# Performance work log

Hardware: AMD Instinct MI355X
Metric: run time of the kernel (lower is better)

The kernel has to match this reference:

```python
import jax, jax.numpy as jnp
import numpy as np

PUPIL = 256          # pupil / OPD grid size
OUTPUT_DIM = 64      # cropped PSF postage-stamp size
N_BINS = 8           # number of SED wavelength bins
BATCH = 16
# Static, wavelength-dependent diffraction padding sizes (phase_N per bin).
# In the original these come from packed_SED_data[:,0,:] but are constant in a FoV.
PHASE_NS = [1024, 988, 952, 918, 886, 856, 828, 802]


def setup_inputs() -> dict:
    key = jax.random.key(0)
    k1, k2, k3 = jax.random.split(key, 3)
    # OPD in meters: small wavefront errors (~lambda/10 rms)
    opd_batch = jax.random.normal(k1, (BATCH, PUPIL, PUPIL), dtype=jnp.float32) * 1e-7
    # Annular pupil: outer aperture with central obscuration (like Euclid/VIS optics)
    yy, xx = np.mgrid[:PUPIL, :PUPIL].astype(np.float32)
    c = (PUPIL - 1) / 2.0
    r = np.sqrt((xx - c) ** 2 + (yy - c) ** 2) / (PUPIL / 2.0)
    obscurations = jnp.asarray(((r <= 1.0) & (r >= 0.3)).astype(np.float32))
    # Observed wavelengths per bin, in meters (visible band)
    lambdas = jnp.linspace(0.55e-6, 0.9e-6, N_BINS).astype(jnp.float32)
    # Normalized SED weights
    sed = jax.random.uniform(k2, (N_BINS,), dtype=jnp.float32) + 0.1
    sed_norms = sed / jnp.sum(sed)
    return {
        "opd_batch": opd_batch,
        "obscurations": obscurations,
        "lambdas": lambdas,
        "sed_norms": sed_norms,
    }


def _mono_psf(opd, obsc, lam, phase_N, out_dim):
    """Batched monochromatic PSF: OPD -> phase -> padded FFT -> cropped |.|^2, unit-sum."""
    # opd: [B, p, p]; phase = exp(i * 2pi/lambda * opd) * obscurations
    pre_phase = (2.0 * jnp.pi / lam) * opd
    phase = (jnp.cos(pre_phase) + 1j * jnp.sin(pre_phase)).astype(jnp.complex64)
    phase = phase * obsc.astype(jnp.complex64)
    p = opd.shape[-1]
    pad_lo = (phase_N - p) // 2
    pad_hi = phase_N - p - pad_lo
    padded = jnp.pad(phase, ((0, 0), (pad_lo, pad_hi), (pad_lo, pad_hi)))  # [B, N, N]
    fft = jnp.fft.fftshift(jnp.fft.fft2(padded), axes=(-2, -1))
    psf = fft.real ** 2 + fft.imag ** 2  # |FFT|^2, float32
    start = phase_N // 2 - out_dim // 2
    psf = psf[:, start:start + out_dim, start:start + out_dim]  # central crop
    return psf / jnp.sum(psf, axis=(-2, -1), keepdims=True)


def reference(opd_batch, obscurations, lambdas, sed_norms):
    # Polychromatic PSF: SED-weighted sum of monochromatic PSFs over wavelength bins.
    # Loop is over the small fixed set of bins (distinct static FFT sizes);
    # each bin is fully vectorized over the batch.
    out = jnp.zeros((opd_batch.shape[0], OUTPUT_DIM, OUTPUT_DIM), dtype=jnp.float32)
    for b, phase_N in enumerate(PHASE_NS):
        out = out + sed_norms[b] * _mono_psf(
            opd_batch, obscurations, lambdas[b], phase_N, OUTPUT_DIM
        )
    return out
```

## Files before the change

### kernel.cpp

```cpp
#include <hip/hip_runtime.h>
#include <math.h>

#define PUPIL 256
#define OUT_DIM 64
#define N_BINS 8
#define BATCH 16

__constant__ int PHASE_NS_C[N_BINS] = {1024, 988, 952, 918, 886, 856, 828, 802};

typedef short bf16x8 __attribute__((ext_vector_type(8)));
typedef float f32x4  __attribute__((ext_vector_type(4)));
typedef int   i32x4  __attribute__((ext_vector_type(4)));

#define MFMA16(a, b, c) __builtin_amdgcn_mfma_f32_16x16x32_bf16((a), (b), (c), 0, 0, 0)

__device__ __forceinline__ short f2bf(float f) {
  unsigned u = __float_as_uint(f);
  u += 0x7FFFu + ((u >> 16) & 1u);
  return (short)(u >> 16);
}

__device__ __forceinline__ bf16x8 neg8(bf16x8 v) {
  i32x4 t = __builtin_bit_cast(i32x4, v);
  t ^= (int)0x80008000;
  return __builtin_bit_cast(bf16x8, t);
}


__global__ void wprep(short* __restrict__ Wr_t, short* __restrict__ Wi_t) {
  int idx = blockIdx.x * 256 + threadIdx.x;
  int n   = idx & 255;
  int k   = (idx >> 8) & 63;
  int bin = idx >> 14;
  int N = PHASE_NS_C[bin];
  int m = ((k - 32) * n) % N;
  if (m < 0) m += N;
  float ang = -6.283185307179586f * (float)m / (float)N;
  float s, c;
  sincosf(ang, &s, &c);
  Wr_t[idx] = f2bf(c);
  Wi_t[idx] = f2bf(s);
}

__global__ __launch_bounds__(256, 2) void stage1(
    const float* __restrict__ opd, const float* __restrict__ obsc,
    const float* __restrict__ lambdas,
    const short* __restrict__ Wr_t, const short* __restrict__ Wi_t,
    short* __restrict__ Gr_t, short* __restrict__ Gi_t)
{
  const int tid = threadIdx.x;
  const int yb = blockIdx.x, bin = blockIdx.y, b = blockIdx.z;
  const int bb = b * N_BINS + bin;
  const float w0 = 6.283185307179586f / lambdas[bin];

  __shared__ short Pr[64 * 32], Pi[64 * 32];

  const int wave = tid >> 6, lane = tid & 63;
  const int lr = lane & 15, lq = lane >> 4;

  f32x4 accR[4], accI[4];
  #pragma unroll
  for (int t = 0; t < 4; ++t) { accR[t] = (f32x4)0.0f; accI[t] = (f32x4)0.0f; }

  const int py = tid >> 2;
  const int px = (tid & 3) * 8;
  const float* opdrow = opd + ((size_t)b * PUPIL + (yb * 64 + py)) * PUPIL;
  const float* obsrow = obsc + (size_t)(yb * 64 + py) * PUPIL;

  const short* wrb = Wr_t + ((size_t)bin * 64 + wave * 16 + lr) * 256 + lq * 8;
  const short* wib = Wi_t + ((size_t)bin * 64 + wave * 16 + lr) * 256 + lq * 8;

  for (int xc = 0; xc < 8; ++xc) {
    const int xbase = xc * 32;
    float od[8], ob[8];
    *(float4*)&od[0] = *(const float4*)(opdrow + xbase + px);
    *(float4*)&od[4] = *(const float4*)(opdrow + xbase + px + 4);
    *(float4*)&ob[0] = *(const float4*)(obsrow + xbase + px);
    *(float4*)&ob[4] = *(const float4*)(obsrow + xbase + px + 4);
    bf16x8 vr, vi;
    #pragma unroll
    for (int j = 0; j < 8; ++j) {
      float s, c;
      __sincosf(w0 * od[j], &s, &c);
      vr[j] = f2bf(c * ob[j]);
      vi[j] = f2bf(s * ob[j]);
    }
    __syncthreads();
    *(bf16x8*)&Pr[py * 32 + px] = vr;
    *(bf16x8*)&Pi[py * 32 + px] = vi;
    const bf16x8 wr  = *(const bf16x8*)(wrb + xbase);
    const bf16x8 wi  = *(const bf16x8*)(wib + xbase);
    const bf16x8 nwi = neg8(wi);
    __syncthreads();

    #pragma unroll
    for (int t = 0; t < 4; ++t) {
      const bf16x8 pr = *(const bf16x8*)&Pr[(t * 16 + lr) * 32 + lq * 8];
      const bf16x8 pi = *(const bf16x8*)&Pi[(t * 16 + lr) * 32 + lq * 8];
      accR[t] = MFMA16(wr,  pr, accR[t]);
      accR[t] = MFMA16(nwi, pi, accR[t]);
      accI[t] = MFMA16(wr,  pi, accI[t]);
      accI[t] = MFMA16(wi,  pr, accI[t]);
    }
  }

  #pragma unroll
  for (int t = 0; t < 4; ++t) {
    const int yg = yb * 64 + t * 16 + lr;
    #pragma unroll
    for (int r = 0; r < 4; ++r) {
      const int kv = wave * 16 + lq * 4 + r;
      const size_t o = ((size_t)bb * 64 + kv) * 256 + yg;
      Gr_t[o] = f2bf(accR[t][r]);
      Gi_t[o] = f2bf(accI[t][r]);
    }
  }
}

__global__ __launch_bounds__(256, 2) void stage2(
    const short* __restrict__ Wr_t, const short* __restrict__ Wi_t,
    const short* __restrict__ Gr_t, const short* __restrict__ Gi_t,
    const float* __restrict__ sed, float* __restrict__ psf_s)
{
  const int tid = threadIdx.x;
  const int bin = blockIdx.x, b = blockIdx.y;
  const int bb = b * N_BINS + bin;

  __shared__ float red[4];

  const int wave = tid >> 6, lane = tid & 63;
  const int lr = lane & 15, lq = lane >> 4;

  f32x4 hr[4], hi[4];
  #pragma unroll
  for (int t = 0; t < 4; ++t) { hr[t] = (f32x4)0.0f; hi[t] = (f32x4)0.0f; }

  const short* grb = Gr_t + ((size_t)bb * 64 + wave * 16 + lr) * 256 + lq * 8;
  const short* gib = Gi_t + ((size_t)bb * 64 + wave * 16 + lr) * 256 + lq * 8;

  for (int yc = 0; yc < 8; ++yc) {
    const int ybase = yc * 32;
    const bf16x8 gr  = *(const bf16x8*)(grb + ybase);
    const bf16x8 gi  = *(const bf16x8*)(gib + ybase);
    const bf16x8 ngi = neg8(gi);
    #pragma unroll
    for (int t = 0; t < 4; ++t) {
      const size_t wo = ((size_t)bin * 64 + t * 16 + lr) * 256 + ybase + lq * 8;
      const bf16x8 wr = *(const bf16x8*)(Wr_t + wo);
      const bf16x8 wi = *(const bf16x8*)(Wi_t + wo);
      hr[t] = MFMA16(gr,  wr, hr[t]);
      hr[t] = MFMA16(ngi, wi, hr[t]);
      hi[t] = MFMA16(gr,  wi, hi[t]);
      hi[t] = MFMA16(gi,  wr, hi[t]);
    }
  }

  float pv[4][4];
  float lsum = 0.f;
  #pragma unroll
  for (int t = 0; t < 4; ++t)
    #pragma unroll
    for (int r = 0; r < 4; ++r) {
      pv[t][r] = hr[t][r] * hr[t][r] + hi[t][r] * hi[t][r];
      lsum += pv[t][r];
    }
  #pragma unroll
  for (int off = 32; off > 0; off >>= 1) lsum += __shfl_down(lsum, off);
  if (lane == 0) red[wave] = lsum;
  __syncthreads();
  const float S = red[0] + red[1] + red[2] + red[3];
  const float scale = sed[bin] / S;

  #pragma unroll
  for (int t = 0; t < 4; ++t) {
    const int u = t * 16 + lr;
    #pragma unroll
    for (int r = 0; r < 4; ++r) {
      const int v = wave * 16 + lq * 4 + r;
      psf_s[(size_t)bb * 4096 + u * 64 + v] = pv[t][r] * scale;
    }
  }
}

__global__ void combine(const float* __restrict__ psf_s, float* __restrict__ out) {
  int idx = blockIdx.x * 256 + threadIdx.x;
  int b = idx >> 12, p = idx & 4095;
  float acc = 0.f;
  #pragma unroll
  for (int bin = 0; bin < N_BINS; ++bin)
    acc += psf_s[(size_t)(b * N_BINS + bin) * 4096 + p];
  out[idx] = acc;
}

extern "C" void kernel_launch(void* const* d_in, const int* in_sizes, int n_in,
                              void* d_out, int out_size, void* d_ws, size_t ws_size,
                              hipStream_t stream) {
  const float* opd     = (const float*)d_in[0];
  const float* obsc    = (const float*)d_in[1];
  const float* lambdas = (const float*)d_in[2];
  const float* sed     = (const float*)d_in[3];
  float* out = (float*)d_out;

  short* Wr_t = (short*)d_ws;
  short* Wi_t = Wr_t + (size_t)N_BINS * 64 * 256;
  short* Gr_t = Wi_t + (size_t)N_BINS * 64 * 256;
  short* Gi_t = Gr_t + (size_t)BATCH * N_BINS * 64 * 256;
  float* psf_s = (float*)(Gi_t + (size_t)BATCH * N_BINS * 64 * 256);

  wprep<<<512, 256, 0, stream>>>(Wr_t, Wi_t);
  stage1<<<dim3(4, N_BINS, BATCH), 256, 0, stream>>>(opd, obsc, lambdas,
                                                     Wr_t, Wi_t, Gr_t, Gi_t);
  stage2<<<dim3(N_BINS, BATCH), 256, 0, stream>>>(Wr_t, Wi_t, Gr_t, Gi_t,
                                                  sed, psf_s);
  combine<<<256, 256, 0, stream>>>(psf_s, out);
}
```

Baseline: 89.04 us.

## Fuse both DFT stages into one kernel with shared-memory intermediate

Merges stage1 and stage2 into one kernel. Each block covers one (batch, bin) pair and one half of the output k-columns. It computes the full 256-row first DFT for its 32 k-values, keeps the intermediate in LDS rather than global memory, and then runs the second DFT. Normalization moves into combine, which uses partial sums written per half. This removes the global round trip for G and one launch, at the cost of recomputing the phase (sincos) twice per (batch, bin), a smaller grid of 256 blocks at occupancy 1, and much larger LDS use.

```diff
diff --git a/kernel.cpp b/kernel.cpp
--- a/kernel.cpp
+++ b/kernel.cpp
@@ -2,7 +2,6 @@
 #include <math.h>
 
 #define PUPIL 256
-#define OUT_DIM 64
 #define N_BINS 8
 #define BATCH 16
 
@@ -19,7 +18,6 @@
   u += 0x7FFFu + ((u >> 16) & 1u);
   return (short)(u >> 16);
 }
-
 __device__ __forceinline__ bf16x8 neg8(bf16x8 v) {
   i32x4 t = __builtin_bit_cast(i32x4, v);
   t ^= (int)0x80008000;
@@ -42,154 +40,172 @@
   Wi_t[idx] = f2bf(s);
 }
 
-__global__ __launch_bounds__(256, 2) void stage1(
+__global__ __launch_bounds__(256, 1) void fused(
     const float* __restrict__ opd, const float* __restrict__ obsc,
     const float* __restrict__ lambdas,
     const short* __restrict__ Wr_t, const short* __restrict__ Wi_t,
-    short* __restrict__ Gr_t, short* __restrict__ Gi_t)
+    float* __restrict__ psf_raw, float* __restrict__ sums)
 {
   const int tid = threadIdx.x;
-  const int yb = blockIdx.x, bin = blockIdx.y, b = blockIdx.z;
+  const int khalf = blockIdx.x, bin = blockIdx.y, b = blockIdx.z;
   const int bb = b * N_BINS + bin;
   const float w0 = 6.283185307179586f / lambdas[bin];
 
-  __shared__ short Pr[64 * 32], Pi[64 * 32];
+  __shared__ short Pr[256 * 40], Pi[256 * 40];
+  __shared__ short Gr[32 * 264], Gi[32 * 264];
+  __shared__ float pvbuf[64 * 33];
+  __shared__ float red[4];
 
   const int wave = tid >> 6, lane = tid & 63;
   const int lr = lane & 15, lq = lane >> 4;
 
-  f32x4 accR[4], accI[4];
-  #pragma unroll
-  for (int t = 0; t < 4; ++t) { accR[t] = (f32x4)0.0f; accI[t] = (f32x4)0.0f; }
-
-  const int py = tid >> 2;
-  const int px = (tid & 3) * 8;
-  const float* opdrow = opd + ((size_t)b * PUPIL + (yb * 64 + py)) * PUPIL;
-  const float* obsrow = obsc + (size_t)(yb * 64 + py) * PUPIL;
-
-  const short* wrb = Wr_t + ((size_t)bin * 64 + wave * 16 + lr) * 256 + lq * 8;
-  const short* wib = Wi_t + ((size_t)bin * 64 + wave * 16 + lr) * 256 + lq * 8;
+  f32x4 aR[2][4], aI[2][4];
+  #pragma unroll
+  for (int m = 0; m < 2; ++m)
+    #pragma unroll
+    for (int t = 0; t < 4; ++t) { aR[m][t] = (f32x4)0.0f; aI[m][t] = (f32x4)0.0f; }
+
+  const int gy0 = tid >> 2;
+  const int gx  = (tid & 3) * 8;
+  const short* wr0 = Wr_t + ((size_t)bin * 64 + khalf * 32 + lr) * 256 + lq * 8;
+  const short* wi0 = Wi_t + ((size_t)bin * 64 + khalf * 32 + lr) * 256 + lq * 8;
 
   for (int xc = 0; xc < 8; ++xc) {
-    const int xbase = xc * 32;
-    float od[8], ob[8];
-    *(float4*)&od[0] = *(const float4*)(opdrow + xbase + px);
-    *(float4*)&od[4] = *(const float4*)(opdrow + xbase + px + 4);
-    *(float4*)&ob[0] = *(const float4*)(obsrow + xbase + px);
-    *(float4*)&ob[4] = *(const float4*)(obsrow + xbase + px + 4);
-    bf16x8 vr, vi;
-    #pragma unroll
-    for (int j = 0; j < 8; ++j) {
-      float s, c;
-      __sincosf(w0 * od[j], &s, &c);
-      vr[j] = f2bf(c * ob[j]);
-      vi[j] = f2bf(s * ob[j]);
+    const int xb = xc * 32;
+    bf16x8 vr[4], vi[4];
+    #pragma unroll
+    for (int i = 0; i < 4; ++i) {
+      const int y = gy0 + i * 64;
+      const float* orow = opd + ((size_t)b * PUPIL + y) * PUPIL + xb + gx;
+      const float* brow = obsc + (size_t)y * PUPIL + xb + gx;
+      float od[8], ob[8];
+      *(float4*)&od[0] = *(const float4*)orow;
+      *(float4*)&od[4] = *(const float4*)(orow + 4);
+      *(float4*)&ob[0] = *(const float4*)brow;
+      *(float4*)&ob[4] = *(const float4*)(brow + 4);
+      #pragma unroll
+      for (int j = 0; j < 8; ++j) {
+        float s, c;
+        __sincosf(w0 * od[j], &s, &c);
+        vr[i][j] = f2bf(c * ob[j]);
+        vi[i][j] = f2bf(s * ob[j]);
+      }
     }
     __syncthreads();
-    *(bf16x8*)&Pr[py * 32 + px] = vr;
-    *(bf16x8*)&Pi[py * 32 + px] = vi;
-    const bf16x8 wr  = *(const bf16x8*)(wrb + xbase);
-    const bf16x8 wi  = *(const bf16x8*)(wib + xbase);
-    const bf16x8 nwi = neg8(wi);
+    #pragma unroll
+    for (int i = 0; i < 4; ++i) {
+      const int y = gy0 + i * 64;
+      *(bf16x8*)&Pr[y * 40 + gx] = vr[i];
+      *(bf16x8*)&Pi[y * 40 + gx] = vi[i];
+    }
+    const bf16x8 w_r0  = *(const bf16x8*)(wr0 + xb);
+    const bf16x8 w_r1  = *(const bf16x8*)(wr0 + 16 * 256 + xb);
+    const bf16x8 w_i0  = *(const bf16x8*)(wi0 + xb);
+    const bf16x8 w_i1  = *(const bf16x8*)(wi0 + 16 * 256 + xb);
+    const bf16x8 nw_i0 = neg8(w_i0);
+    const bf16x8 nw_i1 = neg8(w_i1);
     __syncthreads();
 
-    #pragma unroll
     for (int t = 0; t < 4; ++t) {
-      const bf16x8 pr = *(const bf16x8*)&Pr[(t * 16 + lr) * 32 + lq * 8];
-      const bf16x8 pi = *(const bf16x8*)&Pi[(t * 16 + lr) * 32 + lq * 8];
-      accR[t] = MFMA16(wr,  pr, accR[t]);
-      accR[t] = MFMA16(nwi, pi, accR[t]);
-      accI[t] = MFMA16(wr,  pi, accI[t]);
-      accI[t] = MFMA16(wi,  pr, accI[t]);
-    }
-  }
-
-  #pragma unroll
-  for (int t = 0; t < 4; ++t) {
-    const int yg = yb * 64 + t * 16 + lr;
+      const int y = wave * 64 + t * 16 + lr;
+      const bf16x8 pr = *(const bf16x8*)&Pr[y * 40 + lq * 8];
+      const bf16x8 pi = *(const bf16x8*)&Pi[y * 40 + lq * 8];
+      aR[0][t] = MFMA16(w_r0,  pr, aR[0][t]);
+      aR[0][t] = MFMA16(nw_i0, pi, aR[0][t]);
+      aI[0][t] = MFMA16(w_r0,  pi, aI[0][t]);
+      aI[0][t] = MFMA16(w_i0,  pr, aI[0][t]);
+      aR[1][t] = MFMA16(w_r1,  pr, aR[1][t]);
+      aR[1][t] = MFMA16(nw_i1, pi, aR[1][t]);
+      aI[1][t] = MFMA16(w_r1,  pi, aI[1][t]);
+      aI[1][t] = MFMA16(w_i1,  pr, aI[1][t]);
+    }
+  }
+
+  #pragma unroll
+  for (int m = 0; m < 2; ++m)
+    #pragma unroll
+    for (int t = 0; t < 4; ++t) {
+      const int y = wave * 64 + t * 16 + lr;
+      #pragma unroll
+      for (int r = 0; r < 4; ++r) {
+        const int kvl = m * 16 + lq * 4 + r;
+        Gr[kvl * 264 + y] = f2bf(aR[m][t][r]);
+        Gi[kvl * 264 + y] = f2bf(aI[m][t][r]);
+      }
+    }
+  __syncthreads();
+
+  f32x4 hR[2], hI[2];
+  hR[0] = (f32x4)0.0f; hR[1] = (f32x4)0.0f;
+  hI[0] = (f32x4)0.0f; hI[1] = (f32x4)0.0f;
+
+  for (int yc = 0; yc < 8; ++yc) {
+    const int yb2 = yc * 32;
+    const size_t wo = ((size_t)bin * 64 + wave * 16 + lr) * 256 + yb2 + lq * 8;
+    const bf16x8 w_r = *(const bf16x8*)(Wr_t + wo);
+    const bf16x8 w_i = *(const bf16x8*)(Wi_t + wo);
+    #pragma unroll
+    for (int m = 0; m < 2; ++m) {
+      const bf16x8 g_r = *(const bf16x8*)&Gr[(m * 16 + lr) * 264 + yb2 + lq * 8];
+      const bf16x8 g_i = *(const bf16x8*)&Gi[(m * 16 + lr) * 264 + yb2 + lq * 8];
+      const bf16x8 ng_i = neg8(g_i);
+      hR[m] = MFMA16(g_r,  w_r, hR[m]);
+      hR[m] = MFMA16(ng_i, w_i, hR[m]);
+      hI[m] = MFMA16(g_r,  w_i, hI[m]);
+      hI[m] = MFMA16(g_i,  w_r, hI[m]);
+    }
+  }
+
+  float pv[2][4];
+  float lsum = 0.f;
+  #pragma unroll
+  for (int m = 0; m < 2; ++m)
     #pragma unroll
     for (int r = 0; r < 4; ++r) {
-      const int kv = wave * 16 + lq * 4 + r;
-      const size_t o = ((size_t)bb * 64 + kv) * 256 + yg;
-      Gr_t[o] = f2bf(accR[t][r]);
-      Gi_t[o] = f2bf(accI[t][r]);
-    }
-  }
-}
-
-__global__ __launch_bounds__(256, 2) void stage2(
-    const short* __restrict__ Wr_t, const short* __restrict__ Wi_t,
-    const short* __restrict__ Gr_t, const short* __restrict__ Gi_t,
-    const float* __restrict__ sed, float* __restrict__ psf_s)
-{
-  const int tid = threadIdx.x;
-  const int bin = blockIdx.x, b = blockIdx.y;
-  const int bb = b * N_BINS + bin;
-
-  __shared__ float red[4];
-
-  const int wave = tid >> 6, lane = tid & 63;
-  const int lr = lane & 15, lq = lane >> 4;
-
-  f32x4 hr[4], hi[4];
-  #pragma unroll
-  for (int t = 0; t < 4; ++t) { hr[t] = (f32x4)0.0f; hi[t] = (f32x4)0.0f; }
-
-  const short* grb = Gr_t + ((size_t)bb * 64 + wave * 16 + lr) * 256 + lq * 8;
-  const short* gib = Gi_t + ((size_t)bb * 64 + wave * 16 + lr) * 256 + lq * 8;
-
-  for (int yc = 0; yc < 8; ++yc) {
-    const int ybase = yc * 32;
-    const bf16x8 gr  = *(const bf16x8*)(grb + ybase);
-    const bf16x8 gi  = *(const bf16x8*)(gib + ybase);
-    const bf16x8 ngi = neg8(gi);
-    #pragma unroll
-    for (int t = 0; t < 4; ++t) {
-      const size_t wo = ((size_t)bin * 64 + t * 16 + lr) * 256 + ybase + lq * 8;
-      const bf16x8 wr = *(const bf16x8*)(Wr_t + wo);
-      const bf16x8 wi = *(const bf16x8*)(Wi_t + wo);
-      hr[t] = MFMA16(gr,  wr, hr[t]);
-      hr[t] = MFMA16(ngi, wi, hr[t]);
-      hi[t] = MFMA16(gr,  wi, hi[t]);
-      hi[t] = MFMA16(gi,  wr, hi[t]);
-    }
-  }
-
-  float pv[4][4];
-  float lsum = 0.f;
-  #pragma unroll
-  for (int t = 0; t < 4; ++t)
-    #pragma unroll
-    for (int r = 0; r < 4; ++r) {
-      pv[t][r] = hr[t][r] * hr[t][r] + hi[t][r] * hi[t][r];
-      lsum += pv[t][r];
+      pv[m][r] = hR[m][r] * hR[m][r] + hI[m][r] * hI[m][r];
+      lsum += pv[m][r];
     }
   #pragma unroll
   for (int off = 32; off > 0; off >>= 1) lsum += __shfl_down(lsum, off);
   if (lane == 0) red[wave] = lsum;
+
+  const int u = wave * 16 + lr;
+  #pragma unroll
+  for (int m = 0; m < 2; ++m)
+    #pragma unroll
+    for (int r = 0; r < 4; ++r)
+      pvbuf[u * 33 + m * 16 + lq * 4 + r] = pv[m][r];
   __syncthreads();
-  const float S = red[0] + red[1] + red[2] + red[3];
-  const float scale = sed[bin] / S;
-
-  #pragma unroll
-  for (int t = 0; t < 4; ++t) {
-    const int u = t * 16 + lr;
-    #pragma unroll
-    for (int r = 0; r < 4; ++r) {
-      const int v = wave * 16 + lq * 4 + r;
-      psf_s[(size_t)bb * 4096 + u * 64 + v] = pv[t][r] * scale;
-    }
-  }
-}
-
-__global__ void combine(const float* __restrict__ psf_s, float* __restrict__ out) {
-  int idx = blockIdx.x * 256 + threadIdx.x;
-  int b = idx >> 12, p = idx & 4095;
+
+  if (tid == 0)
+    sums[bb * 2 + khalf] = red[0] + red[1] + red[2] + red[3];
+
+  #pragma unroll
+  for (int k2 = 0; k2 < 8; ++k2) {
+    const int i = tid + k2 * 256;
+    const int uu = i >> 5, vl = i & 31;
+    psf_raw[(size_t)bb * 4096 + uu * 64 + khalf * 32 + vl] = pvbuf[uu * 33 + vl];
+  }
+}
+
+__global__ void combine(const float* __restrict__ psf_raw,
+                        const float* __restrict__ sums,
+                        const float* __restrict__ sed,
+                        float* __restrict__ out) {
+  __shared__ float sc[N_BINS];
+  const int blk = blockIdx.x;
+  const int b = blk >> 4;
+  const int px = (blk & 15) * 256 + threadIdx.x;
+  if (threadIdx.x < N_BINS) {
+    const int bb = b * N_BINS + threadIdx.x;
+    sc[threadIdx.x] = sed[threadIdx.x] / (sums[bb * 2] + sums[bb * 2 + 1]);
+  }
+  __syncthreads();
   float acc = 0.f;
   #pragma unroll
   for (int bin = 0; bin < N_BINS; ++bin)
-    acc += psf_s[(size_t)(b * N_BINS + bin) * 4096 + p];
-  out[idx] = acc;
+    acc += sc[bin] * psf_raw[(size_t)(b * N_BINS + bin) * 4096 + px];
+  out[b * 4096 + px] = acc;
 }
 
 extern "C" void kernel_launch(void* const* d_in, const int* in_sizes, int n_in,
@@ -201,16 +217,13 @@
   const float* sed     = (const float*)d_in[3];
   float* out = (float*)d_out;
 
-  short* Wr_t = (short*)d_ws;
-  short* Wi_t = Wr_t + (size_t)N_BINS * 64 * 256;
-  short* Gr_t = Wi_t + (size_t)N_BINS * 64 * 256;
-  short* Gi_t = Gr_t + (size_t)BATCH * N_BINS * 64 * 256;
-  float* psf_s = (float*)(Gi_t + (size_t)BATCH * N_BINS * 64 * 256);
+  short* Wr_t   = (short*)d_ws;
+  short* Wi_t   = Wr_t + (size_t)N_BINS * 64 * 256;
+  float* psf_raw = (float*)(Wi_t + (size_t)N_BINS * 64 * 256);
+  float* sums    = psf_raw + (size_t)BATCH * N_BINS * 4096;
 
   wprep<<<512, 256, 0, stream>>>(Wr_t, Wi_t);
-  stage1<<<dim3(4, N_BINS, BATCH), 256, 0, stream>>>(opd, obsc, lambdas,
-                                                     Wr_t, Wi_t, Gr_t, Gi_t);
-  stage2<<<dim3(N_BINS, BATCH), 256, 0, stream>>>(Wr_t, Wi_t, Gr_t, Gi_t,
-                                                  sed, psf_s);
-  combine<<<256, 256, 0, stream>>>(psf_s, out);
-}
+  fused<<<dim3(2, N_BINS, BATCH), 256, 0, stream>>>(opd, obsc, lambdas,
+                                                    Wr_t, Wi_t, psf_raw, sums);
+  combine<<<256, 256, 0, stream>>>(psf_raw, sums, sed, out);
+}
```

Measured after the change: 84.98 us. 1.05x faster.

## Split stage1/stage2 across more blocks and defer PSF normalisation to combine

Applied to the files above, without the earlier changes.

Stage1 now handles 32 pupil rows per block instead of 64, doubling its grid to 1024 blocks. Stage2 splits the 64 output rows into four 16-row blocks, writes unnormalised intensities through a padded shared-memory transpose for coalesced stores, and emits per-block partial sums. The combine kernel finishes the per-bin normalisation and SED weighting. The intent is to fill more compute units than the original 128-block stage2 grid did, at the cost of an extra sums buffer, more total blocks, and the twiddle table switching to the fast __sincosf.

```diff
diff --git a/kernel.cpp b/kernel.cpp
--- a/kernel.cpp
+++ b/kernel.cpp
@@ -2,13 +2,13 @@
 #include <math.h>
 
 #define PUPIL 256
-#define OUT_DIM 64
 #define N_BINS 8
 #define BATCH 16
 
 __constant__ int PHASE_NS_C[N_BINS] = {1024, 988, 952, 918, 886, 856, 828, 802};
 
 typedef short bf16x8 __attribute__((ext_vector_type(8)));
+typedef short bf16x4 __attribute__((ext_vector_type(4)));
 typedef float f32x4  __attribute__((ext_vector_type(4)));
 typedef int   i32x4  __attribute__((ext_vector_type(4)));
 
@@ -19,7 +19,6 @@
   u += 0x7FFFu + ((u >> 16) & 1u);
   return (short)(u >> 16);
 }
-
 __device__ __forceinline__ bf16x8 neg8(bf16x8 v) {
   i32x4 t = __builtin_bit_cast(i32x4, v);
   t ^= (int)0x80008000;
@@ -37,159 +36,162 @@
   if (m < 0) m += N;
   float ang = -6.283185307179586f * (float)m / (float)N;
   float s, c;
-  sincosf(ang, &s, &c);
+  __sincosf(ang, &s, &c);
   Wr_t[idx] = f2bf(c);
   Wi_t[idx] = f2bf(s);
 }
 
-__global__ __launch_bounds__(256, 2) void stage1(
+__global__ __launch_bounds__(256, 4) void stage1(
     const float* __restrict__ opd, const float* __restrict__ obsc,
     const float* __restrict__ lambdas,
     const short* __restrict__ Wr_t, const short* __restrict__ Wi_t,
     short* __restrict__ Gr_t, short* __restrict__ Gi_t)
 {
   const int tid = threadIdx.x;
-  const int yb = blockIdx.x, bin = blockIdx.y, b = blockIdx.z;
+  const int yb = blockIdx.x * 32, bin = blockIdx.y, b = blockIdx.z;
   const int bb = b * N_BINS + bin;
   const float w0 = 6.283185307179586f / lambdas[bin];
 
-  __shared__ short Pr[64 * 32], Pi[64 * 32];
+  __shared__ short Pr[32 * 32], Pi[32 * 32];
 
   const int wave = tid >> 6, lane = tid & 63;
   const int lr = lane & 15, lq = lane >> 4;
 
-  f32x4 accR[4], accI[4];
-  #pragma unroll
-  for (int t = 0; t < 4; ++t) { accR[t] = (f32x4)0.0f; accI[t] = (f32x4)0.0f; }
-
-  const int py = tid >> 2;
-  const int px = (tid & 3) * 8;
-  const float* opdrow = opd + ((size_t)b * PUPIL + (yb * 64 + py)) * PUPIL;
-  const float* obsrow = obsc + (size_t)(yb * 64 + py) * PUPIL;
-
+  f32x4 aR[2], aI[2];
+  aR[0] = (f32x4)0.0f; aR[1] = (f32x4)0.0f;
+  aI[0] = (f32x4)0.0f; aI[1] = (f32x4)0.0f;
+
+  const int gy = tid >> 3;
+  const int gx = (tid & 7) * 4;
+  const float* orow = opd + ((size_t)b * PUPIL + yb + gy) * PUPIL;
+  const float* brow = obsc + (size_t)(yb + gy) * PUPIL;
   const short* wrb = Wr_t + ((size_t)bin * 64 + wave * 16 + lr) * 256 + lq * 8;
   const short* wib = Wi_t + ((size_t)bin * 64 + wave * 16 + lr) * 256 + lq * 8;
 
   for (int xc = 0; xc < 8; ++xc) {
-    const int xbase = xc * 32;
-    float od[8], ob[8];
-    *(float4*)&od[0] = *(const float4*)(opdrow + xbase + px);
-    *(float4*)&od[4] = *(const float4*)(opdrow + xbase + px + 4);
-    *(float4*)&ob[0] = *(const float4*)(obsrow + xbase + px);
-    *(float4*)&ob[4] = *(const float4*)(obsrow + xbase + px + 4);
-    bf16x8 vr, vi;
-    #pragma unroll
-    for (int j = 0; j < 8; ++j) {
+    const int xb = xc * 32;
+    const float4 od = *(const float4*)(orow + xb + gx);
+    const float4 ob = *(const float4*)(brow + xb + gx);
+    bf16x4 vr, vi;
+    {
       float s, c;
-      __sincosf(w0 * od[j], &s, &c);
-      vr[j] = f2bf(c * ob[j]);
-      vi[j] = f2bf(s * ob[j]);
+      __sincosf(w0 * od.x, &s, &c); vr[0] = f2bf(c * ob.x); vi[0] = f2bf(s * ob.x);
+      __sincosf(w0 * od.y, &s, &c); vr[1] = f2bf(c * ob.y); vi[1] = f2bf(s * ob.y);
+      __sincosf(w0 * od.z, &s, &c); vr[2] = f2bf(c * ob.z); vi[2] = f2bf(s * ob.z);
+      __sincosf(w0 * od.w, &s, &c); vr[3] = f2bf(c * ob.w); vi[3] = f2bf(s * ob.w);
     }
     __syncthreads();
-    *(bf16x8*)&Pr[py * 32 + px] = vr;
-    *(bf16x8*)&Pi[py * 32 + px] = vi;
-    const bf16x8 wr  = *(const bf16x8*)(wrb + xbase);
-    const bf16x8 wi  = *(const bf16x8*)(wib + xbase);
-    const bf16x8 nwi = neg8(wi);
+    *(bf16x4*)&Pr[gy * 32 + gx] = vr;
+    *(bf16x4*)&Pi[gy * 32 + gx] = vi;
+    const bf16x8 w_r  = *(const bf16x8*)(wrb + xb);
+    const bf16x8 w_i  = *(const bf16x8*)(wib + xb);
+    const bf16x8 nw_i = neg8(w_i);
     __syncthreads();
 
-    #pragma unroll
-    for (int t = 0; t < 4; ++t) {
+    for (int t = 0; t < 2; ++t) {
       const bf16x8 pr = *(const bf16x8*)&Pr[(t * 16 + lr) * 32 + lq * 8];
       const bf16x8 pi = *(const bf16x8*)&Pi[(t * 16 + lr) * 32 + lq * 8];
-      accR[t] = MFMA16(wr,  pr, accR[t]);
-      accR[t] = MFMA16(nwi, pi, accR[t]);
-      accI[t] = MFMA16(wr,  pi, accI[t]);
-      accI[t] = MFMA16(wi,  pr, accI[t]);
+      aR[t] = MFMA16(w_r,  pr, aR[t]);
+      aR[t] = MFMA16(nw_i, pi, aR[t]);
+      aI[t] = MFMA16(w_r,  pi, aI[t]);
+      aI[t] = MFMA16(w_i,  pr, aI[t]);
     }
   }
 
   #pragma unroll
-  for (int t = 0; t < 4; ++t) {
-    const int yg = yb * 64 + t * 16 + lr;
+  for (int t = 0; t < 2; ++t) {
+    const int y = yb + t * 16 + lr;
     #pragma unroll
     for (int r = 0; r < 4; ++r) {
       const int kv = wave * 16 + lq * 4 + r;
-      const size_t o = ((size_t)bb * 64 + kv) * 256 + yg;
-      Gr_t[o] = f2bf(accR[t][r]);
-      Gi_t[o] = f2bf(accI[t][r]);
+      const size_t o = ((size_t)bb * 64 + kv) * 256 + y;
+      Gr_t[o] = f2bf(aR[t][r]);
+      Gi_t[o] = f2bf(aI[t][r]);
     }
   }
 }
 
-__global__ __launch_bounds__(256, 2) void stage2(
+__global__ __launch_bounds__(256, 4) void stage2(
     const short* __restrict__ Wr_t, const short* __restrict__ Wi_t,
     const short* __restrict__ Gr_t, const short* __restrict__ Gi_t,
-    const float* __restrict__ sed, float* __restrict__ psf_s)
+    float* __restrict__ psf_raw, float* __restrict__ sums)
 {
   const int tid = threadIdx.x;
-  const int bin = blockIdx.x, b = blockIdx.y;
+  const int uc = blockIdx.x, bin = blockIdx.y, b = blockIdx.z;
   const int bb = b * N_BINS + bin;
 
+  __shared__ float pvbuf[64 * 17];
   __shared__ float red[4];
 
   const int wave = tid >> 6, lane = tid & 63;
   const int lr = lane & 15, lq = lane >> 4;
 
-  f32x4 hr[4], hi[4];
-  #pragma unroll
-  for (int t = 0; t < 4; ++t) { hr[t] = (f32x4)0.0f; hi[t] = (f32x4)0.0f; }
+  f32x4 hR = (f32x4)0.0f, hI = (f32x4)0.0f;
 
   const short* grb = Gr_t + ((size_t)bb * 64 + wave * 16 + lr) * 256 + lq * 8;
   const short* gib = Gi_t + ((size_t)bb * 64 + wave * 16 + lr) * 256 + lq * 8;
+  const short* wrb = Wr_t + ((size_t)bin * 64 + uc * 16 + lr) * 256 + lq * 8;
+  const short* wib = Wi_t + ((size_t)bin * 64 + uc * 16 + lr) * 256 + lq * 8;
 
   for (int yc = 0; yc < 8; ++yc) {
-    const int ybase = yc * 32;
-    const bf16x8 gr  = *(const bf16x8*)(grb + ybase);
-    const bf16x8 gi  = *(const bf16x8*)(gib + ybase);
-    const bf16x8 ngi = neg8(gi);
-    #pragma unroll
-    for (int t = 0; t < 4; ++t) {
-      const size_t wo = ((size_t)bin * 64 + t * 16 + lr) * 256 + ybase + lq * 8;
-      const bf16x8 wr = *(const bf16x8*)(Wr_t + wo);
-      const bf16x8 wi = *(const bf16x8*)(Wi_t + wo);
-      hr[t] = MFMA16(gr,  wr, hr[t]);
-      hr[t] = MFMA16(ngi, wi, hr[t]);
-      hi[t] = MFMA16(gr,  wi, hi[t]);
-      hi[t] = MFMA16(gi,  wr, hi[t]);
-    }
-  }
-
-  float pv[4][4];
-  float lsum = 0.f;
-  #pragma unroll
-  for (int t = 0; t < 4; ++t)
-    #pragma unroll
-    for (int r = 0; r < 4; ++r) {
-      pv[t][r] = hr[t][r] * hr[t][r] + hi[t][r] * hi[t][r];
-      lsum += pv[t][r];
-    }
+    const int yb = yc * 32;
+    const bf16x8 g_r  = *(const bf16x8*)(grb + yb);
+    const bf16x8 g_i  = *(const bf16x8*)(gib + yb);
+    const bf16x8 w_r  = *(const bf16x8*)(wrb + yb);
+    const bf16x8 w_i  = *(const bf16x8*)(wib + yb);
+    const bf16x8 ng_i = neg8(g_i);
+    hR = MFMA16(g_r,  w_r, hR);
+    hR = MFMA16(ng_i, w_i, hR);
+    hI = MFMA16(g_r,  w_i, hI);
+    hI = MFMA16(g_i,  w_r, hI);
+  }
+
+  float pv[4], lsum = 0.f;
+  #pragma unroll
+  for (int r = 0; r < 4; ++r) {
+    pv[r] = hR[r] * hR[r] + hI[r] * hI[r];
+    lsum += pv[r];
+  }
   #pragma unroll
   for (int off = 32; off > 0; off >>= 1) lsum += __shfl_down(lsum, off);
   if (lane == 0) red[wave] = lsum;
+
+  #pragma unroll
+  for (int r = 0; r < 4; ++r)
+    pvbuf[(wave * 16 + lq * 4 + r) * 17 + lr] = pv[r];
   __syncthreads();
-  const float S = red[0] + red[1] + red[2] + red[3];
-  const float scale = sed[bin] / S;
-
-  #pragma unroll
-  for (int t = 0; t < 4; ++t) {
-    const int u = t * 16 + lr;
-    #pragma unroll
-    for (int r = 0; r < 4; ++r) {
-      const int v = wave * 16 + lq * 4 + r;
-      psf_s[(size_t)bb * 4096 + u * 64 + v] = pv[t][r] * scale;
-    }
-  }
-}
-
-__global__ void combine(const float* __restrict__ psf_s, float* __restrict__ out) {
-  int idx = blockIdx.x * 256 + threadIdx.x;
-  int b = idx >> 12, p = idx & 4095;
+
+  if (tid == 0)
+    sums[bb * 4 + uc] = red[0] + red[1] + red[2] + red[3];
+
+  #pragma unroll
+  for (int it = 0; it < 4; ++it) {
+    const int i  = tid + it * 256;
+    const int ul = i >> 6;
+    const int v  = i & 63;
+    psf_raw[(size_t)bb * 4096 + (uc * 16 + ul) * 64 + v] = pvbuf[v * 17 + ul];
+  }
+}
+
+__global__ void combine(const float* __restrict__ psf_raw,
+                        const float* __restrict__ sums,
+                        const float* __restrict__ sed,
+                        float* __restrict__ out) {
+  __shared__ float sc[N_BINS];
+  const int blk = blockIdx.x;
+  const int b = blk >> 4;
+  const int px = (blk & 15) * 256 + threadIdx.x;
+  if (threadIdx.x < N_BINS) {
+    const int bb = b * N_BINS + threadIdx.x;
+    const float S = sums[bb * 4] + sums[bb * 4 + 1] + sums[bb * 4 + 2] + sums[bb * 4 + 3];
+    sc[threadIdx.x] = sed[threadIdx.x] / S;
+  }
+  __syncthreads();
   float acc = 0.f;
   #pragma unroll
   for (int bin = 0; bin < N_BINS; ++bin)
-    acc += psf_s[(size_t)(b * N_BINS + bin) * 4096 + p];
-  out[idx] = acc;
+    acc += sc[bin] * psf_raw[(size_t)(b * N_BINS + bin) * 4096 + px];
+  out[b * 4096 + px] = acc;
 }
 
 extern "C" void kernel_launch(void* const* d_in, const int* in_sizes, int n_in,
@@ -205,12 +207,13 @@
   short* Wi_t = Wr_t + (size_t)N_BINS * 64 * 256;
   short* Gr_t = Wi_t + (size_t)N_BINS * 64 * 256;
   short* Gi_t = Gr_t + (size_t)BATCH * N_BINS * 64 * 256;
-  float* psf_s = (float*)(Gi_t + (size_t)BATCH * N_BINS * 64 * 256);
+  float* psf_raw = (float*)(Gi_t + (size_t)BATCH * N_BINS * 64 * 256);
+  float* sums    = psf_raw + (size_t)BATCH * N_BINS * 4096;
 
   wprep<<<512, 256, 0, stream>>>(Wr_t, Wi_t);
-  stage1<<<dim3(4, N_BINS, BATCH), 256, 0, stream>>>(opd, obsc, lambdas,
+  stage1<<<dim3(8, N_BINS, BATCH), 256, 0, stream>>>(opd, obsc, lambdas,
                                                      Wr_t, Wi_t, Gr_t, Gi_t);
-  stage2<<<dim3(N_BINS, BATCH), 256, 0, stream>>>(Wr_t, Wi_t, Gr_t, Gi_t,
-                                                  sed, psf_s);
-  combine<<<256, 256, 0, stream>>>(psf_s, out);
-}
+  stage2<<<dim3(4, N_BINS, BATCH), 256, 0, stream>>>(Wr_t, Wi_t, Gr_t, Gi_t,
+                                                     psf_raw, sums);
+  combine<<<256, 256, 0, stream>>>(psf_raw, sums, sed, out);
+}
```

Result: no change. 88.18 us (-1.0%).
